# Kernel optimization log

Measured on AMD Instinct MI355X. Metric: run time of the kernel, lower is better.

Reference implementation:

```python
import jax, jax.numpy as jnp
import numpy as np

BETA = 5.5
MEM_FILLED = 25  # number of occupied slots per class; remaining slots are zero (empty)


def setup_inputs() -> dict:
    key = jax.random.key(0)
    ks = jax.random.split(key, 7)
    C, M, D = 1000, 50, 1024
    mem = jax.random.normal(ks[0], (C, M, D), jnp.float32)
    # emulate a partially-filled memory bank: slots >= MEM_FILLED are empty (all-zero rows)
    mem = mem * (jnp.arange(M)[None, :, None] < MEM_FILLED)
    return {
        "img_feat": jax.random.normal(ks[1], (1, D), jnp.float32),
        "image_feature_memory": mem,
        "fixed_global_feat_vanilla": jax.random.normal(ks[2], (C, 1, D), jnp.float32),
        "global_bias": 0.01 * jax.random.normal(ks[3], (C, D), jnp.float32),
        "global_bias_key": 0.01 * jax.random.normal(ks[4], (C, D), jnp.float32),
        "global_bias_value": 0.01 * jax.random.normal(ks[5], (C, D), jnp.float32),
        "global_ffn_bias": 0.01 * jax.random.normal(ks[6], (C, D), jnp.float32),
        "logit_scale": jnp.asarray(np.log(100.0), dtype=jnp.float32),
    }


def _l2norm(x, axis=-1):
    return x / jnp.linalg.norm(x, axis=axis, keepdims=True)


def reference(img_feat, image_feature_memory, fixed_global_feat_vanilla,
              global_bias, global_bias_key, global_bias_value,
              global_ffn_bias, logit_scale):
    # DualMem.get_image_pred, args.position == 'all', similarity_weighted classifier
    sg = jax.lax.stop_gradient  # torch.no_grad() block
    mem = jnp.concatenate([image_feature_memory, fixed_global_feat_vanilla], axis=1)  # (C, M+1, D)

    q = img_feat + jnp.mean(global_bias, axis=0, keepdims=True)      # (1, D)
    K = mem + global_bias_key[:, None, :]                             # (C, M+1, D)
    V = mem + global_bias_value[:, None, :]                           # (C, M+1, D)

    empty = (jnp.sum(mem, axis=-1) == 0)[..., None]                   # (C, M+1, 1) empty slots
    Kn = jnp.where(empty, 0.0, _l2norm(K))
    Vn = jnp.where(empty, 0.0, _l2norm(V))
    qn = _l2norm(q)
    qn, Kn, Vn = sg(qn), sg(Kn), sg(Vn)

    sim = jnp.exp(-BETA * (1.0 - jnp.einsum('d,cmd->cm', qn[0], Kn)))  # (C, M+1)
    adaptive = jnp.einsum('cm,cmd->cd', sim, Vn)                       # (C, D)
    adaptive = _l2norm(adaptive)
    adaptive = adaptive[None] + global_ffn_bias[None]                  # (1, C, D) position in {'output','all'}
    adaptive = _l2norm(adaptive)

    logits = jnp.exp(logit_scale) * jnp.einsum('bcd,bd->bc', adaptive, img_feat)  # (1, C)
    return jax.nn.softmax(logits, axis=1)
```

## Files before the change

kernel.cpp:

```cpp
#include <hip/hip_runtime.h>
#include <math.h>

#define BETA 5.5f
#define NC 1000
#define NM 51
#define ND 1024

typedef float nt_float4 __attribute__((ext_vector_type(4)));

__device__ __forceinline__ float wave_reduce_sum(float v) {
#pragma unroll
    for (int off = 32; off >= 1; off >>= 1) v += __shfl_xor(v, off, 64);
    return v;
}

__device__ __forceinline__ float block_reduce_sum(float v, float* red, int w, int lane) {
    v = wave_reduce_sum(v);
    __syncthreads();
    if (lane == 0) red[w] = v;
    __syncthreads();
    return red[0] + red[1] + red[2] + red[3];
}

__global__ __launch_bounds__(128) void colsum_kernel(const float* __restrict__ gb,
                                                     float* __restrict__ qpart) {
    int d = blockIdx.x * 128 + threadIdx.x;
    int c0 = blockIdx.y * 125;
    const float* p = gb + (size_t)c0 * ND + d;
    float s = 0.f;
    for (int c = 0; c < 125; ++c) s += p[(size_t)c * ND];
    qpart[blockIdx.y * ND + d] = s;
}

__global__ __launch_bounds__(256) void dualmem_main(
    const float* __restrict__ img,
    const float* __restrict__ mem,
    const float* __restrict__ fixedg,
    const float* __restrict__ qpart,
    const float* __restrict__ gbk,
    const float* __restrict__ gbv,
    float* __restrict__ accpart)
{
    __shared__ float lds_acc[4 * ND];

    const int c = blockIdx.x >> 1;
    const int half = blockIdx.x & 1;
    const int t = threadIdx.x;
    const int w = t >> 6;
    const int lane = t & 63;
    const int ww = half * 4 + w;

    float4 qn[4];
    float ssq = 0.f;
#pragma unroll
    for (int j = 0; j < 4; ++j) {
        float4 sv = make_float4(0.f, 0.f, 0.f, 0.f);
#pragma unroll
        for (int p = 0; p < 8; ++p) {
            float4 pv = ((const float4*)qpart)[p * 256 + j * 64 + lane];
            sv.x += pv.x; sv.y += pv.y; sv.z += pv.z; sv.w += pv.w;
        }
        float4 iv = ((const float4*)img)[j * 64 + lane];
        float4 qv;
        qv.x = iv.x + sv.x * (1.f / NC);
        qv.y = iv.y + sv.y * (1.f / NC);
        qv.z = iv.z + sv.z * (1.f / NC);
        qv.w = iv.w + sv.w * (1.f / NC);
        ssq += qv.x * qv.x + qv.y * qv.y + qv.z * qv.z + qv.w * qv.w;
        qn[j] = qv;
    }
    ssq = wave_reduce_sum(ssq);
    float qrn = rsqrtf(ssq);
#pragma unroll
    for (int j = 0; j < 4; ++j) {
        qn[j].x *= qrn; qn[j].y *= qrn; qn[j].z *= qrn; qn[j].w *= qrn;
    }

    const float* bkp = gbk + (size_t)c * ND;
    const float* bvp = gbv + (size_t)c * ND;
    float4 bk[4], bv[4], acc[4];
#pragma unroll
    for (int j = 0; j < 4; ++j) {
        bk[j] = ((const float4*)bkp)[j * 64 + lane];
        bv[j] = ((const float4*)bvp)[j * 64 + lane];
        acc[j] = make_float4(0.f, 0.f, 0.f, 0.f);
    }

    for (int m = ww; m < NM; m += 8) {
        const nt_float4* row = (m < 50) ? (const nt_float4*)(mem + ((size_t)c * 50 + m) * ND)
                                        : (const nt_float4*)(fixedg + (size_t)c * ND);
        nt_float4 mv[4];
        float sm = 0.f, ssqK = 0.f, dotK = 0.f, ssqV = 0.f;
#pragma unroll
        for (int j = 0; j < 4; ++j) {
            nt_float4 v = __builtin_nontemporal_load(&row[j * 64 + lane]);
            mv[j] = v;
            sm += v.x + v.y + v.z + v.w;
            float kx = v.x + bk[j].x, ky = v.y + bk[j].y, kz = v.z + bk[j].z, kw = v.w + bk[j].w;
            ssqK += kx * kx + ky * ky + kz * kz + kw * kw;
            dotK += qn[j].x * kx + qn[j].y * ky + qn[j].z * kz + qn[j].w * kw;
            float vx = v.x + bv[j].x, vy = v.y + bv[j].y, vz = v.z + bv[j].z, vw = v.w + bv[j].w;
            ssqV += vx * vx + vy * vy + vz * vz + vw * vw;
        }
        sm   = wave_reduce_sum(sm);
        ssqK = wave_reduce_sum(ssqK);
        dotK = wave_reduce_sum(dotK);
        ssqV = wave_reduce_sum(ssqV);
        if (sm != 0.f) {
            float simv = expf(-BETA * (1.f - dotK * rsqrtf(ssqK)));
            float wt = simv * rsqrtf(ssqV);
#pragma unroll
            for (int j = 0; j < 4; ++j) {
                acc[j].x += wt * (mv[j].x + bv[j].x);
                acc[j].y += wt * (mv[j].y + bv[j].y);
                acc[j].z += wt * (mv[j].z + bv[j].z);
                acc[j].w += wt * (mv[j].w + bv[j].w);
            }
        }
    }

#pragma unroll
    for (int j = 0; j < 4; ++j)
        ((float4*)lds_acc)[w * 256 + j * 64 + lane] = acc[j];
    __syncthreads();

    float4 a = make_float4(0.f, 0.f, 0.f, 0.f);
#pragma unroll
    for (int wv = 0; wv < 4; ++wv) {
        float4 p = ((float4*)lds_acc)[wv * 256 + t];
        a.x += p.x; a.y += p.y; a.z += p.z; a.w += p.w;
    }
    ((float4*)(accpart + (size_t)blockIdx.x * ND))[t] = a;
}

__global__ __launch_bounds__(256) void finalize_kernel(
    const float* __restrict__ img,
    const float* __restrict__ accpart,
    const float* __restrict__ ffn,
    const float* __restrict__ lsp,
    float* __restrict__ logits)
{
    __shared__ float red[8];
    const int c = blockIdx.x;
    const int t = threadIdx.x;
    const int w = t >> 6;
    const int lane = t & 63;

    float4 a0 = ((const float4*)(accpart + (size_t)(2 * c) * ND))[t];
    float4 a1 = ((const float4*)(accpart + (size_t)(2 * c + 1) * ND))[t];
    float4 a;
    a.x = a0.x + a1.x; a.y = a0.y + a1.y; a.z = a0.z + a1.z; a.w = a0.w + a1.w;

    float ssqA = block_reduce_sum(a.x * a.x + a.y * a.y + a.z * a.z + a.w * a.w, red, w, lane);
    float arn = rsqrtf(ssqA);
    float4 fv = ((const float4*)(ffn + (size_t)c * ND))[t];
    a.x = a.x * arn + fv.x;
    a.y = a.y * arn + fv.y;
    a.z = a.z * arn + fv.z;
    a.w = a.w * arn + fv.w;
    float ssqB = block_reduce_sum(a.x * a.x + a.y * a.y + a.z * a.z + a.w * a.w, red, w, lane);
    float brn = rsqrtf(ssqB);

    float4 iv = ((const float4*)img)[t];
    float dp = a.x * iv.x + a.y * iv.y + a.z * iv.z + a.w * iv.w;
    dp = block_reduce_sum(dp, red, w, lane);

    if (t == 0) logits[c] = expf(lsp[0]) * dp * brn;
}

__global__ __launch_bounds__(256) void softmax_kernel(const float* __restrict__ logits,
                                                      float* __restrict__ out) {
    __shared__ float red[8];
    int t = threadIdx.x, w = t >> 6, lane = t & 63;
    float l[4];
#pragma unroll
    for (int i = 0; i < 4; ++i) {
        int idx = t * 4 + i;
        l[i] = (idx < NC) ? logits[idx] : -3.402823466e+38f;
    }
    float mx = fmaxf(fmaxf(l[0], l[1]), fmaxf(l[2], l[3]));
#pragma unroll
    for (int off = 32; off >= 1; off >>= 1) mx = fmaxf(mx, __shfl_xor(mx, off, 64));
    __syncthreads();
    if (lane == 0) red[w] = mx;
    __syncthreads();
    mx = fmaxf(fmaxf(red[0], red[1]), fmaxf(red[2], red[3]));
    __syncthreads();

    float e[4], s = 0.f;
#pragma unroll
    for (int i = 0; i < 4; ++i) {
        int idx = t * 4 + i;
        e[i] = (idx < NC) ? expf(l[i] - mx) : 0.f;
        s += e[i];
    }
    s = block_reduce_sum(s, red, w, lane);
    float inv = 1.f / s;
#pragma unroll
    for (int i = 0; i < 4; ++i) {
        int idx = t * 4 + i;
        if (idx < NC) out[idx] = e[i] * inv;
    }
}

extern "C" void kernel_launch(void* const* d_in, const int* in_sizes, int n_in,
                              void* d_out, int out_size, void* d_ws, size_t ws_size,
                              hipStream_t stream) {
    const float* img    = (const float*)d_in[0];
    const float* mem    = (const float*)d_in[1];
    const float* fixedg = (const float*)d_in[2];
    const float* gb     = (const float*)d_in[3];
    const float* gbk    = (const float*)d_in[4];
    const float* gbv    = (const float*)d_in[5];
    const float* ffn    = (const float*)d_in[6];
    const float* ls     = (const float*)d_in[7];

    float* ws      = (float*)d_ws;
    float* qpart   = ws;
    float* accpart = ws + 8 * ND;
    float* logits  = accpart + 2000 * ND;
    float* out     = (float*)d_out;

    colsum_kernel<<<dim3(8, 8), 128, 0, stream>>>(gb, qpart);
    dualmem_main<<<2 * NC, 256, 0, stream>>>(img, mem, fixedg, qpart, gbk, gbv, accpart);
    finalize_kernel<<<NC, 256, 0, stream>>>(img, accpart, ffn, ls, logits);
    softmax_kernel<<<1, 256, 0, stream>>>(logits, out);
}
```

Measured before the change: 318.7 us.

## Precompute normalized query once and fuse softmax into finalize via last-block atomic

The query normalization that every main-kernel block recomputed from the eight column-sum partials is moved into the last block of the column-sum kernel, chosen by an atomic counter, and written once as qn. The main kernel then only loads the 4 KB normalized query. The softmax kernel is folded into the finalize kernel: the last block to finish, again found with an atomic counter, computes the softmax, which removes one launch. A memset of the counters is added per call, along with threadfences and the serial tail work of the last block.

```diff
diff --git a/kernel.cpp b/kernel.cpp
--- a/kernel.cpp
+++ b/kernel.cpp
@@ -14,7 +14,7 @@
     return v;
 }
 
-__device__ __forceinline__ float block_reduce_sum(float v, float* red, int w, int lane) {
+__device__ __forceinline__ float block_reduce_sum4(float v, float* red, int w, int lane) {
     v = wave_reduce_sum(v);
     __syncthreads();
     if (lane == 0) red[w] = v;
@@ -22,21 +22,62 @@
     return red[0] + red[1] + red[2] + red[3];
 }
 
-__global__ __launch_bounds__(128) void colsum_kernel(const float* __restrict__ gb,
-                                                     float* __restrict__ qpart) {
-    int d = blockIdx.x * 128 + threadIdx.x;
-    int c0 = blockIdx.y * 125;
+__global__ __launch_bounds__(128) void colsum_qn_kernel(
+    const float* __restrict__ gb, const float* __restrict__ img,
+    float* __restrict__ qpart, float* __restrict__ qn, int* __restrict__ cnt) {
+    __shared__ int flag;
+    __shared__ float red2[2];
+    const int t = threadIdx.x;
+    const int d = blockIdx.x * 128 + t;
+    const int c0 = blockIdx.y * 125;
     const float* p = gb + (size_t)c0 * ND + d;
     float s = 0.f;
     for (int c = 0; c < 125; ++c) s += p[(size_t)c * ND];
     qpart[blockIdx.y * ND + d] = s;
+
+    __threadfence();
+    __syncthreads();
+    if (t == 0) flag = (atomicAdd(&cnt[0], 1) == 63);
+    __syncthreads();
+    if (!flag) return;
+    __threadfence();
+
+    float4 q[2];
+    float ssq = 0.f;
+#pragma unroll
+    for (int h = 0; h < 2; ++h) {
+        const int idx = t + h * 128;
+        float4 sv = make_float4(0.f, 0.f, 0.f, 0.f);
+#pragma unroll
+        for (int pp = 0; pp < 8; ++pp) {
+            float4 pv = ((const float4*)qpart)[pp * 256 + idx];
+            sv.x += pv.x; sv.y += pv.y; sv.z += pv.z; sv.w += pv.w;
+        }
+        float4 iv = ((const float4*)img)[idx];
+        q[h].x = iv.x + sv.x * (1.f / NC);
+        q[h].y = iv.y + sv.y * (1.f / NC);
+        q[h].z = iv.z + sv.z * (1.f / NC);
+        q[h].w = iv.w + sv.w * (1.f / NC);
+        ssq += q[h].x * q[h].x + q[h].y * q[h].y + q[h].z * q[h].z + q[h].w * q[h].w;
+    }
+    ssq = wave_reduce_sum(ssq);
+    const int lane = t & 63, w = t >> 6;
+    if (lane == 0) red2[w] = ssq;
+    __syncthreads();
+    const float r = rsqrtf(red2[0] + red2[1]);
+#pragma unroll
+    for (int h = 0; h < 2; ++h) {
+        const int idx = t + h * 128;
+        float4 o;
+        o.x = q[h].x * r; o.y = q[h].y * r; o.z = q[h].z * r; o.w = q[h].w * r;
+        ((float4*)qn)[idx] = o;
+    }
 }
 
 __global__ __launch_bounds__(256) void dualmem_main(
-    const float* __restrict__ img,
     const float* __restrict__ mem,
     const float* __restrict__ fixedg,
-    const float* __restrict__ qpart,
+    const float* __restrict__ qnv,
     const float* __restrict__ gbk,
     const float* __restrict__ gbv,
     float* __restrict__ accpart)
@@ -51,30 +92,8 @@
     const int ww = half * 4 + w;
 
     float4 qn[4];
-    float ssq = 0.f;
-#pragma unroll
-    for (int j = 0; j < 4; ++j) {
-        float4 sv = make_float4(0.f, 0.f, 0.f, 0.f);
-#pragma unroll
-        for (int p = 0; p < 8; ++p) {
-            float4 pv = ((const float4*)qpart)[p * 256 + j * 64 + lane];
-            sv.x += pv.x; sv.y += pv.y; sv.z += pv.z; sv.w += pv.w;
-        }
-        float4 iv = ((const float4*)img)[j * 64 + lane];
-        float4 qv;
-        qv.x = iv.x + sv.x * (1.f / NC);
-        qv.y = iv.y + sv.y * (1.f / NC);
-        qv.z = iv.z + sv.z * (1.f / NC);
-        qv.w = iv.w + sv.w * (1.f / NC);
-        ssq += qv.x * qv.x + qv.y * qv.y + qv.z * qv.z + qv.w * qv.w;
-        qn[j] = qv;
-    }
-    ssq = wave_reduce_sum(ssq);
-    float qrn = rsqrtf(ssq);
-#pragma unroll
-    for (int j = 0; j < 4; ++j) {
-        qn[j].x *= qrn; qn[j].y *= qrn; qn[j].z *= qrn; qn[j].w *= qrn;
-    }
+#pragma unroll
+    for (int j = 0; j < 4; ++j) qn[j] = ((const float4*)qnv)[j * 64 + lane];
 
     const float* bkp = gbk + (size_t)c * ND;
     const float* bvp = gbv + (size_t)c * ND;
@@ -138,9 +157,12 @@
     const float* __restrict__ accpart,
     const float* __restrict__ ffn,
     const float* __restrict__ lsp,
-    float* __restrict__ logits)
+    float* __restrict__ logits,
+    int* __restrict__ cnt,
+    float* __restrict__ out)
 {
     __shared__ float red[8];
+    __shared__ int flag;
     const int c = blockIdx.x;
     const int t = threadIdx.x;
     const int w = t >> 6;
@@ -151,27 +173,29 @@
     float4 a;
     a.x = a0.x + a1.x; a.y = a0.y + a1.y; a.z = a0.z + a1.z; a.w = a0.w + a1.w;
 
-    float ssqA = block_reduce_sum(a.x * a.x + a.y * a.y + a.z * a.z + a.w * a.w, red, w, lane);
+    float ssqA = block_reduce_sum4(a.x * a.x + a.y * a.y + a.z * a.z + a.w * a.w, red, w, lane);
     float arn = rsqrtf(ssqA);
     float4 fv = ((const float4*)(ffn + (size_t)c * ND))[t];
     a.x = a.x * arn + fv.x;
     a.y = a.y * arn + fv.y;
     a.z = a.z * arn + fv.z;
     a.w = a.w * arn + fv.w;
-    float ssqB = block_reduce_sum(a.x * a.x + a.y * a.y + a.z * a.z + a.w * a.w, red, w, lane);
+    float ssqB = block_reduce_sum4(a.x * a.x + a.y * a.y + a.z * a.z + a.w * a.w, red, w, lane);
     float brn = rsqrtf(ssqB);
 
     float4 iv = ((const float4*)img)[t];
     float dp = a.x * iv.x + a.y * iv.y + a.z * iv.z + a.w * iv.w;
-    dp = block_reduce_sum(dp, red, w, lane);
+    dp = block_reduce_sum4(dp, red, w, lane);
 
     if (t == 0) logits[c] = expf(lsp[0]) * dp * brn;
-}
-
-__global__ __launch_bounds__(256) void softmax_kernel(const float* __restrict__ logits,
-                                                      float* __restrict__ out) {
-    __shared__ float red[8];
-    int t = threadIdx.x, w = t >> 6, lane = t & 63;
+
+    __threadfence();
+    __syncthreads();
+    if (t == 0) flag = (atomicAdd(&cnt[1], 1) == NC - 1);
+    __syncthreads();
+    if (!flag) return;
+    __threadfence();
+
     float l[4];
 #pragma unroll
     for (int i = 0; i < 4; ++i) {
@@ -185,7 +209,6 @@
     if (lane == 0) red[w] = mx;
     __syncthreads();
     mx = fmaxf(fmaxf(red[0], red[1]), fmaxf(red[2], red[3]));
-    __syncthreads();
 
     float e[4], s = 0.f;
 #pragma unroll
@@ -194,7 +217,7 @@
         e[i] = (idx < NC) ? expf(l[i] - mx) : 0.f;
         s += e[i];
     }
-    s = block_reduce_sum(s, red, w, lane);
+    s = block_reduce_sum4(s, red, w, lane);
     float inv = 1.f / s;
 #pragma unroll
     for (int i = 0; i < 4; ++i) {
@@ -217,12 +240,14 @@
 
     float* ws      = (float*)d_ws;
     float* qpart   = ws;
-    float* accpart = ws + 8 * ND;
+    float* qn      = qpart + 8 * ND;
+    float* accpart = qn + ND;
     float* logits  = accpart + 2000 * ND;
+    int*   cnt     = (int*)(logits + NC);
     float* out     = (float*)d_out;
 
-    colsum_kernel<<<dim3(8, 8), 128, 0, stream>>>(gb, qpart);
-    dualmem_main<<<2 * NC, 256, 0, stream>>>(img, mem, fixedg, qpart, gbk, gbv, accpart);
-    finalize_kernel<<<NC, 256, 0, stream>>>(img, accpart, ffn, ls, logits);
-    softmax_kernel<<<1, 256, 0, stream>>>(logits, out);
-}
+    hipMemsetAsync(cnt, 0, 2 * sizeof(int), stream);
+    colsum_qn_kernel<<<dim3(8, 8), 128, 0, stream>>>(gb, img, qpart, qn, cnt);
+    dualmem_main<<<2 * NC, 256, 0, stream>>>(mem, fixedg, qn, gbk, gbv, accpart);
+    finalize_kernel<<<NC, 256, 0, stream>>>(img, accpart, ffn, ls, logits, cnt, out);
+}
```

Result: slower. 378.4 us (+18.8%).
